# Kernel optimization log

Measured on AMD Instinct MI355X. Metric: run time of the kernel, lower is better.

The kernel has to match this reference:

```python
import jax, jax.numpy as jnp
import numpy as np
import math

SR = 16000
FFT = 1024
WIN = 640
HOP = 320
NMEL = 40
NCEP = 13
B = 1024
NS = 16000
F_MIN = 0.0
F_MAX = 8000.0
LIFT_L = 22.0
DELTA_N = 2


def _linear_to_mel_weight_matrix(num_mel, num_spec_bins, sr, fmin, fmax):
    # Exact replica of tf.signal.linear_to_mel_weight_matrix (HTK mel scale).
    def hz_to_mel(f):
        return 1127.0 * np.log1p(np.asarray(f, np.float64) / 700.0)
    nyquist = sr / 2.0
    lin_freqs = np.linspace(0.0, nyquist, num_spec_bins)
    spec_mel = hz_to_mel(lin_freqs[1:])[:, None]          # drop DC bin
    edges = np.linspace(hz_to_mel(fmin), hz_to_mel(fmax), num_mel + 2)
    lower, center, upper = edges[:-2], edges[1:-1], edges[2:]
    lower_slope = (spec_mel - lower) / (center - lower)
    upper_slope = (upper - spec_mel) / (upper - center)
    w = np.maximum(0.0, np.minimum(lower_slope, upper_slope))
    w = np.pad(w, ((1, 0), (0, 0)))                       # re-add zero DC row
    return w.astype(np.float32)


def setup_inputs() -> dict:
    key = jax.random.key(0)
    waveforms = jax.random.normal(key, (B, NS), dtype=jnp.float32)
    mel_fb = jnp.asarray(_linear_to_mel_weight_matrix(NMEL, FFT // 2 + 1, SR, F_MIN, F_MAX))
    return {"waveforms": waveforms, "mel_fb": mel_fb}


def _delta(feat, N):
    # feat: (B, T, C). Replicate-pad N frames at both ends, then weighted
    # sliding-window sum with weights k in [-N..N] (vectorized, no map_fn).
    T = feat.shape[1]
    denom = 2.0 * sum(float(k * k) for k in range(1, N + 1))
    padded = jnp.concatenate(
        [jnp.repeat(feat[:, :1, :], N, axis=1), feat,
         jnp.repeat(feat[:, -1:, :], N, axis=1)], axis=1)
    acc = jnp.zeros_like(feat)
    for k in range(-N, N + 1):
        if k != 0:
            acc = acc + float(k) * padded[:, N + k:N + k + T, :]
    return acc / denom


def reference(waveforms, mel_fb):
    # --- STFT (tf.signal.stft: periodic Hann, no pad_end, zero-pad to FFT) ---
    n = jnp.arange(WIN, dtype=jnp.float32)
    window = 0.5 - 0.5 * jnp.cos(2.0 * math.pi * n / WIN)
    num_frames = 1 + (NS - WIN) // HOP                    # 49
    idx = jnp.arange(num_frames)[:, None] * HOP + jnp.arange(WIN)[None, :]
    frames = waveforms[:, idx] * window
    frames = jnp.pad(frames, ((0, 0), (0, 0), (0, FFT - WIN)))
    spec = jnp.abs(jnp.fft.rfft(frames, n=FFT, axis=-1))  # (B, T, 513)

    # --- mel + log ---
    log_mel = jnp.log(spec @ mel_fb + 1e-6)               # (B, T, NMEL)

    # --- MFCC: DCT-II scaled by rsqrt(2*NMEL), keep first NCEP coeffs ---
    m = jnp.arange(NMEL, dtype=jnp.float32)[:, None]
    k = jnp.arange(NCEP, dtype=jnp.float32)[None, :]
    dct_mat = 2.0 * jnp.cos(math.pi * (2.0 * m + 1.0) * k / (2.0 * NMEL))
    mfccs = (log_mel @ dct_mat) * (1.0 / math.sqrt(2.0 * NMEL))

    # --- liftering ---
    c = jnp.arange(NCEP, dtype=jnp.float32)
    lift = 1.0 + (LIFT_L / 2.0) * jnp.sin(math.pi * c / LIFT_L)
    mfccs = mfccs * lift

    # --- deltas and delta-deltas ---
    d1 = _delta(mfccs, DELTA_N)
    d2 = _delta(d1, DELTA_N)
    out = jnp.concatenate([mfccs, d1, d2], axis=2)        # (B, T, 3*NCEP)
    return out[..., None]                                 # (B, T, 39, 1)
```

## Files before the change

kernel.cpp:

```cpp
#include <hip/hip_runtime.h>
#include <math.h>

#define NMEL   40
#define NCEP   13
#define BATCH  1024
#define NSAMP  16000
#define NFRAME 49
#define PI_F   3.14159265358979323846f

#define WS_WIN  0
#define WS_R    640
#define WS_DT   1664
#define WS_BT   2184
#define WS_TOT  15240

typedef _Float16 half8 __attribute__((ext_vector_type(8)));
typedef __fp16   fp16x2 __attribute__((ext_vector_type(2)));
typedef float f32x4 __attribute__((ext_vector_type(4)));

#define WAVE_FENCE() { __builtin_amdgcn_wave_barrier(); asm volatile("" ::: "memory"); }

#define BFLY(i0, i1, wr, wi) {                        \
    float tr = zr[i0] - zr[i1], ti = zi[i0] - zi[i1]; \
    zr[i0] += zr[i1]; zi[i0] += zi[i1];               \
    zr[i1] = tr*(wr) - ti*(wi);                       \
    zi[i1] = tr*(wi) + ti*(wr); }

__device__ __forceinline__ unsigned pk_f16(float a, float b) {
    fp16x2 h = __builtin_amdgcn_cvt_pkrtz(a, b);
    union { fp16x2 h; unsigned u; } cvt; cvt.h = h;
    return cvt.u;
}

__global__ __launch_bounds__(256) void mfcc_prep(
    const float* __restrict__ mel_fb, float* __restrict__ ws)
{
    const int idx = blockIdx.x * 256 + threadIdx.x;

    _Float16* bt = (_Float16*)(ws + WS_BT);
    for (int i = idx; i < 48 * 544; i += 64 * 256) {
        int n = i / 544, k = i - n * 544;
        float v = (n < NMEL && k < 513) ? mel_fb[k * NMEL + n] : 0.0f;
        bt[i] = (_Float16)v;
    }

    if (idx < 640 + 512 + 520) {
        int i = idx;
        if (i < 640) {
            ws[WS_WIN + i] = 0.5f - 0.5f * cosf(2.0f * PI_F * (float)i / 640.0f);
        } else if (i < 1152) {
            int k = i - 640;
            float s, c;
            sincosf(-2.0f * PI_F * (float)k / 1024.0f, &s, &c);
            ((float2*)(ws + WS_R))[k] = make_float2(c, s);
        } else {
            int j = i - 1152;
            int m = j / 13, c0 = j - m * 13;
            float d    = 2.0f * cosf(PI_F * (2.0f * m + 1.0f) * (float)c0 / 80.0f);
            float lift = 1.0f + 11.0f * sinf(PI_F * (float)c0 / 22.0f);
            ws[WS_DT + j] = d * 0.11180339887498949f * lift;
        }
    }
}

__global__ __launch_bounds__(256) void mfcc_stage1(
    const float* __restrict__ wave, const float* __restrict__ ws,
    float* __restrict__ out)
{
    __shared__ __align__(16) char smem[4 * 576 * 8 + 16 * 40 * 2];
    char* smemc = smem;
    _Float16* lm = (_Float16*)(smem + 4 * 576 * 8);

    const int tid = threadIdx.x;
    const int wv  = tid >> 6;
    const int L   = tid & 63;
    const int s   = L & 7;

    float2* Z = (float2*)smem + wv * 576;
    const float2* R   = (const float2*)(ws + WS_R);
    const float2* win = (const float2*)(ws + WS_WIN);

    float2 twA[4], twB[2], twC, twD[4], twE[2], twF, twS[8], winv[5];
    #pragma unroll
    for (int j = 0; j < 4; ++j) twA[j] = R[2 * (L + 64 * j)];
    #pragma unroll
    for (int j = 0; j < 2; ++j) twB[j] = R[4 * (L + 64 * j)];
    twC = R[8 * L];
    #pragma unroll
    for (int j = 0; j < 4; ++j) twD[j] = R[128 * j + 16 * s];
    #pragma unroll
    for (int j = 0; j < 2; ++j) twE[j] = R[256 * j + 32 * s];
    twF = R[64 * s];
    #pragma unroll
    for (int j = 0; j < 8; ++j) twS[j] = R[8 * L + j];
    #pragma unroll
    for (int j = 0; j < 5; ++j) winv[j] = win[L + 64 * j];

    uint4 mgp[4];
    float m512v[4] = {0.0f, 0.0f, 0.0f, 0.0f};

    #pragma unroll
    for (int fi = 0; fi < 4; ++fi) {
        const int frame = blockIdx.x * 16 + wv * 4 + fi;
        const int b = frame / NFRAME;
        const int f = frame - b * NFRAME;
        const float2* xin = (const float2*)(wave + (size_t)b * NSAMP + (size_t)f * 320);

        float zr[8], zi[8];
        #pragma unroll
        for (int j = 0; j < 8; ++j) { zr[j] = 0.0f; zi[j] = 0.0f; }
        #pragma unroll
        for (int j = 0; j < 5; ++j) {
            float2 x = xin[L + 64 * j];
            zr[j] = x.x * winv[j].x;
            zi[j] = x.y * winv[j].y;
        }

        #pragma unroll
        for (int j = 0; j < 4; ++j) BFLY(j, j + 4, twA[j].x, twA[j].y);
        #pragma unroll
        for (int g = 0; g < 8; g += 4) {
            #pragma unroll
            for (int j = 0; j < 2; ++j) BFLY(g + j, g + j + 2, twB[j].x, twB[j].y);
        }
        #pragma unroll
        for (int i0 = 0; i0 < 8; i0 += 2) BFLY(i0, i0 + 1, twC.x, twC.y);

        WAVE_FENCE();
        #pragma unroll
        for (int j = 0; j < 8; ++j) {
            int n = L + 64 * j;
            Z[n + (n >> 3)] = make_float2(zr[j], zi[j]);
        }
        WAVE_FENCE();
        #pragma unroll
        for (int j = 0; j < 8; ++j) {
            int n = (L >> 3) * 64 + 8 * j + s;
            float2 v = Z[n + (n >> 3)];
            zr[j] = v.x; zi[j] = v.y;
        }

        #pragma unroll
        for (int j = 0; j < 4; ++j) BFLY(j, j + 4, twD[j].x, twD[j].y);
        #pragma unroll
        for (int g = 0; g < 8; g += 4) {
            #pragma unroll
            for (int j = 0; j < 2; ++j) BFLY(g + j, g + j + 2, twE[j].x, twE[j].y);
        }
        #pragma unroll
        for (int i0 = 0; i0 < 8; i0 += 2) BFLY(i0, i0 + 1, twF.x, twF.y);

        WAVE_FENCE();
        #pragma unroll
        for (int j = 0; j < 8; ++j) {
            int n = (L >> 3) * 64 + 8 * j + s;
            Z[n + (n >> 6)] = make_float2(zr[j], zi[j]);
        }
        WAVE_FENCE();
        {
            int base = 8 * L + (L >> 3);
            #pragma unroll
            for (int j = 0; j < 8; ++j) {
                float2 v = Z[base + j];
                zr[j] = v.x; zi[j] = v.y;
            }
        }

        {
            const float C = 0.70710678118654752f;
            const float w8r[4] = { 1.0f,  C, 0.0f, -C };
            const float w8i[4] = { 0.0f, -C, -1.0f, -C };
            #pragma unroll
            for (int j = 0; j < 4; ++j) BFLY(j, j + 4, w8r[j], w8i[j]);
            #pragma unroll
            for (int g = 0; g < 8; g += 4) {
                BFLY(g + 0, g + 2, 1.0f, 0.0f);
                BFLY(g + 1, g + 3, 0.0f, -1.0f);
            }
            #pragma unroll
            for (int i0 = 0; i0 < 8; i0 += 2) BFLY(i0, i0 + 1, 1.0f, 0.0f);
        }

        WAVE_FENCE();
        {
            const int rev3t[8] = { 0, 4, 2, 6, 1, 5, 3, 7 };
            int r6 = (int)(__brev((unsigned)L) >> 26);
            #pragma unroll
            for (int j = 0; j < 8; ++j) {
                int k = rev3t[j] * 64 + r6;
                Z[k + rev3t[j]] = make_float2(zr[j], zi[j]);
            }
        }
        WAVE_FENCE();

        float mg[8];
        #pragma unroll
        for (int j = 0; j < 8; ++j) {
            int k = 8 * L + j;
            if (k == 0) {
                float2 z0 = Z[0];
                mg[j]     = fabsf(z0.x + z0.y);
                m512v[fi] = fabsf(z0.x - z0.y);
            } else {
                int n2 = 512 - k;
                float2 A  = Z[k  + (k  >> 6)];
                float2 Bv = Z[n2 + (n2 >> 6)];
                float xer = 0.5f * (A.x + Bv.x), xei = 0.5f * (A.y - Bv.y);
                float xo  = 0.5f * (A.y + Bv.y), xoi = -0.5f * (A.x - Bv.x);
                float xr = xer + twS[j].x * xo - twS[j].y * xoi;
                float xi = xei + twS[j].x * xoi + twS[j].y * xo;
                mg[j] = sqrtf(xr * xr + xi * xi);
            }
        }
        mgp[fi].x = pk_f16(mg[0], mg[1]);
        mgp[fi].y = pk_f16(mg[2], mg[3]);
        mgp[fi].z = pk_f16(mg[4], mg[5]);
        mgp[fi].w = pk_f16(mg[6], mg[7]);
        WAVE_FENCE();
    }

    __syncthreads();
    #pragma unroll
    for (int fi = 0; fi < 4; ++fi) {
        const int row = wv * 4 + fi;
        *(uint4*)(smemc + row * 1104 + 16 * L) = mgp[fi];
        if (L < 20) {
            unsigned v = (L == 0) ? pk_f16(m512v[fi], 0.0f) : 0u;
            *(unsigned*)(smemc + row * 1104 + 1024 + 4 * L) = v;
        }
    }
    __syncthreads();

    if (wv < 3) {
        const int nl = L & 15, q = L >> 4;
        const char* ap = smemc + nl * 1104 + q * 16;
        const _Float16* btp = (const _Float16*)(ws + WS_BT)
                              + (size_t)(wv * 16 + nl) * 544 + q * 8;
        f32x4 acc = {0.0f, 0.0f, 0.0f, 0.0f};
        #pragma unroll
        for (int kk = 0; kk < 17; ++kk) {
            half8 a = *(const half8*)(ap + kk * 64);
            half8 b = *(const half8*)(btp + kk * 32);
            acc = __builtin_amdgcn_mfma_f32_16x16x32_f16(a, b, acc, 0, 0, 0);
        }
        const int mel = wv * 16 + nl;
        if (mel < NMEL) {
            #pragma unroll
            for (int r = 0; r < 4; ++r) {
                int fl = q * 4 + r;
                lm[fl * NMEL + mel] = (_Float16)__logf(acc[r] + 1e-6f);
            }
        }
    }
    __syncthreads();

    if (tid < 16 * NCEP) {
        const int fl = tid / NCEP, c = tid - fl * NCEP;
        float acc = 0.0f;
        #pragma unroll
        for (int m = 0; m < NMEL; ++m)
            acc += (float)lm[fl * NMEL + m] * ws[WS_DT + m * 13 + c];
        out[(size_t)(blockIdx.x * 16 + fl) * (3 * NCEP) + c] = acc;
    }
}

__global__ __launch_bounds__(128) void mfcc_stage2(float* __restrict__ out)
{
    __shared__ float x [NFRAME * NCEP];
    __shared__ float d1[NFRAME * NCEP];

    const int b = blockIdx.x;
    const int tid = threadIdx.x;
    const int TC = NFRAME * NCEP;

    for (int i = tid; i < TC; i += 128) {
        const int t = i / NCEP, c = i - t * NCEP;
        x[i] = out[((size_t)b * NFRAME + t) * (3 * NCEP) + c];
    }
    __syncthreads();

    for (int i = tid; i < TC; i += 128) {
        const int t = i / NCEP, c = i - t * NCEP;
        float acc = 0.0f;
        #pragma unroll
        for (int k = -2; k <= 2; ++k) {
            if (k == 0) continue;
            int tt = t + k;
            tt = tt < 0 ? 0 : (tt > NFRAME - 1 ? NFRAME - 1 : tt);
            acc += (float)k * x[tt * NCEP + c];
        }
        d1[i] = acc * 0.1f;
    }
    __syncthreads();

    for (int i = tid; i < TC; i += 128) {
        const int t = i / NCEP, c = i - t * NCEP;
        float acc = 0.0f;
        #pragma unroll
        for (int k = -2; k <= 2; ++k) {
            if (k == 0) continue;
            int tt = t + k;
            tt = tt < 0 ? 0 : (tt > NFRAME - 1 ? NFRAME - 1 : tt);
            acc += (float)k * d1[tt * NCEP + c];
        }
        const size_t base = ((size_t)b * NFRAME + t) * (3 * NCEP);
        out[base +     NCEP + c] = d1[i];
        out[base + 2 * NCEP + c] = acc * 0.1f;
    }
}

extern "C" void kernel_launch(void* const* d_in, const int* in_sizes, int n_in,
                              void* d_out, int out_size, void* d_ws, size_t ws_size,
                              hipStream_t stream)
{
    const float* wave   = (const float*)d_in[0];
    const float* mel_fb = (const float*)d_in[1];
    float* out = (float*)d_out;
    float* ws  = (float*)d_ws;

    mfcc_prep<<<64, 256, 0, stream>>>(mel_fb, ws);
    mfcc_stage1<<<(BATCH * NFRAME) / 16, 256, 0, stream>>>(wave, ws, out);
    mfcc_stage2<<<BATCH, 128, 0, stream>>>(out);
}
```

Baseline: 184.5 us.

## Prefetch next frame's samples into registers and move split twiddles to LDS

Loads the next frame's windowed input samples into a second register buffer while the current frame's FFT runs, so global load latency overlaps compute. The eight per-lane post-processing twiddles are no longer held in registers; they are staged once per block into a 512-entry LDS table and read per use. This lowers register pressure to make room for the prefetch buffers, at the cost of an extra block barrier, LDS reads inside the loop, and more shared memory per block.

```diff
diff --git a/kernel.cpp b/kernel.cpp
--- a/kernel.cpp
+++ b/kernel.cpp
@@ -68,6 +68,7 @@
     float* __restrict__ out)
 {
     __shared__ __align__(16) char smem[4 * 576 * 8 + 16 * 40 * 2];
+    __shared__ __align__(16) float2 Rlds[512];
     char* smemc = smem;
     _Float16* lm = (_Float16*)(smem + 4 * 576 * 8);
 
@@ -80,7 +81,10 @@
     const float2* R   = (const float2*)(ws + WS_R);
     const float2* win = (const float2*)(ws + WS_WIN);
 
-    float2 twA[4], twB[2], twC, twD[4], twE[2], twF, twS[8], winv[5];
+    #pragma unroll
+    for (int i = tid; i < 512; i += 256) Rlds[i] = R[i];
+
+    float2 twA[4], twB[2], twC, twD[4], twE[2], twF, winv[5];
     #pragma unroll
     for (int j = 0; j < 4; ++j) twA[j] = R[2 * (L + 64 * j)];
     #pragma unroll
@@ -92,28 +96,43 @@
     for (int j = 0; j < 2; ++j) twE[j] = R[256 * j + 32 * s];
     twF = R[64 * s];
     #pragma unroll
-    for (int j = 0; j < 8; ++j) twS[j] = R[8 * L + j];
-    #pragma unroll
     for (int j = 0; j < 5; ++j) winv[j] = win[L + 64 * j];
+
+    __syncthreads();
 
     uint4 mgp[4];
     float m512v[4] = {0.0f, 0.0f, 0.0f, 0.0f};
 
-    #pragma unroll
-    for (int fi = 0; fi < 4; ++fi) {
-        const int frame = blockIdx.x * 16 + wv * 4 + fi;
+    float2 xb0[5], xb1[5];
+    {
+        const int frame = blockIdx.x * 16 + wv * 4;
         const int b = frame / NFRAME;
         const int f = frame - b * NFRAME;
-        const float2* xin = (const float2*)(wave + (size_t)b * NSAMP + (size_t)f * 320);
+        const float2* p = (const float2*)(wave + (size_t)b * NSAMP + (size_t)f * 320);
+        #pragma unroll
+        for (int j = 0; j < 5; ++j) xb0[j] = p[L + 64 * j];
+    }
+
+    #pragma unroll
+    for (int fi = 0; fi < 4; ++fi) {
+        float2* cur = (fi & 1) ? xb1 : xb0;
+        float2* nxt = (fi & 1) ? xb0 : xb1;
+        if (fi < 3) {
+            const int frame = blockIdx.x * 16 + wv * 4 + fi + 1;
+            const int b = frame / NFRAME;
+            const int f = frame - b * NFRAME;
+            const float2* p = (const float2*)(wave + (size_t)b * NSAMP + (size_t)f * 320);
+            #pragma unroll
+            for (int j = 0; j < 5; ++j) nxt[j] = p[L + 64 * j];
+        }
 
         float zr[8], zi[8];
         #pragma unroll
         for (int j = 0; j < 8; ++j) { zr[j] = 0.0f; zi[j] = 0.0f; }
         #pragma unroll
         for (int j = 0; j < 5; ++j) {
-            float2 x = xin[L + 64 * j];
-            zr[j] = x.x * winv[j].x;
-            zi[j] = x.y * winv[j].y;
+            zr[j] = cur[j].x * winv[j].x;
+            zi[j] = cur[j].y * winv[j].y;
         }
 
         #pragma unroll
@@ -197,6 +216,7 @@
         #pragma unroll
         for (int j = 0; j < 8; ++j) {
             int k = 8 * L + j;
+            float2 wS = Rlds[k & 511];
             if (k == 0) {
                 float2 z0 = Z[0];
                 mg[j]     = fabsf(z0.x + z0.y);
@@ -207,8 +227,8 @@
                 float2 Bv = Z[n2 + (n2 >> 6)];
                 float xer = 0.5f * (A.x + Bv.x), xei = 0.5f * (A.y - Bv.y);
                 float xo  = 0.5f * (A.y + Bv.y), xoi = -0.5f * (A.x - Bv.x);
-                float xr = xer + twS[j].x * xo - twS[j].y * xoi;
-                float xi = xei + twS[j].x * xoi + twS[j].y * xo;
+                float xr = xer + wS.x * xo - wS.y * xoi;
+                float xi = xei + wS.x * xoi + wS.y * xo;
                 mg[j] = sqrtf(xr * xr + xi * xi);
             }
         }
```

After: 188.7 us. 1.02x slower.
